# Kernel tuning notes

Measured on AMD Instinct MI355X. Metric: run time of the kernel, lower is better.

The kernel has to match this reference:

```python
import jax, jax.numpy as jnp
import numpy as np

B = 131072   # batch of states (e.g. ODE integrator batch)
S = 2        # state_dim (q, p)
H = 512      # hidden_dim
E = 8        # action_embedding_dim


def setup_inputs() -> dict:
    key = jax.random.key(0)
    ks = jax.random.split(key, 8)
    sc = lambda n: 1.0 / np.sqrt(n)
    return {
        "t": 0,  # unused time scalar (odeint signature)
        "state": jax.random.normal(ks[0], (B, S), dtype=jnp.float32),
        "action_emb": jax.random.normal(ks[1], (B, E), dtype=jnp.float32),
        # H_net: Linear(S,H) -> Softplus -> Linear(H,H) -> Softplus -> Linear(H,1)
        "W1": jax.random.normal(ks[2], (S, H), dtype=jnp.float32) * sc(S),
        "b1": jnp.zeros((H,), dtype=jnp.float32),
        "W2": jax.random.normal(ks[3], (H, H), dtype=jnp.float32) * sc(H),
        "b2": jnp.zeros((H,), dtype=jnp.float32),
        "W3": jax.random.normal(ks[4], (H, 1), dtype=jnp.float32) * sc(H),
        "b3": jnp.zeros((1,), dtype=jnp.float32),
        "log_damping": jnp.asarray(-1.0, dtype=jnp.float32),
        # G_net: Linear(E, S//2)
        "Gw": jax.random.normal(ks[5], (E, S // 2), dtype=jnp.float32) * sc(E),
        "Gb": jnp.zeros((S // 2,), dtype=jnp.float32),
    }


def reference(t, state, action_emb, W1, b1, W2, b2, W3, b3, log_damping, Gw, Gb):
    # Hamiltonian net: scalar H per state; sum over batch so jax.grad gives
    # per-sample dH/dstate in one pass (equivalent to autograd.grad with ones cotangent).
    def H_sum(s):
        h = jax.nn.softplus(s @ W1 + b1)       # [B, H]
        h = jax.nn.softplus(h @ W2 + b2)       # [B, H]
        return jnp.sum(h @ W3 + b3)            # scalar

    dH_dstate = jax.grad(H_sum)(state)         # [B, S]
    dH_dq = dH_dstate[..., 0:1]                # [B, 1]
    dH_dp = dH_dstate[..., 1:2]                # [B, 1]

    damping = jnp.exp(log_damping)
    G_u = action_emb @ Gw + Gb                 # [B, 1]

    dq_dt = dH_dp
    dp_dt = -dH_dq - damping * dH_dp + G_u
    return jnp.concatenate([dq_dt, dp_dt], axis=-1)  # [B, S]
```

## Files before the change

### kernel.cpp

```cpp
#include <hip/hip_runtime.h>

typedef __bf16 bf16x8 __attribute__((ext_vector_type(8)));
typedef float f32x4 __attribute__((ext_vector_type(4)));
typedef float f32x16 __attribute__((ext_vector_type(16)));
typedef unsigned short u16x8 __attribute__((ext_vector_type(8)));

#define DEVI static __device__ __forceinline__

DEVI unsigned short f2b(float x) {
  __bf16 b = (__bf16)x;
  return __builtin_bit_cast(unsigned short, b);
}

DEVI float ex2(float x) {
#if __has_builtin(__builtin_amdgcn_exp2f)
  return __builtin_amdgcn_exp2f(x);
#else
  return __expf(x * 0.69314718f);
#endif
}
DEVI float lg2(float x) {
#if __has_builtin(__builtin_amdgcn_logf)
  return __builtin_amdgcn_logf(x);
#else
  return __logf(x) * 1.44269504f;
#endif
}

__global__ __launch_bounds__(256) void pack_w2_kernel(
    const float* __restrict__ W2, unsigned short* __restrict__ p1,
    unsigned short* __restrict__ p2) {
  int idx = blockIdx.x * 256 + threadIdx.x;
  int which = idx >> 18;
  int i = idx & 262143;
  int j = i & 7;
  int l = (i >> 3) & 63;
  if (which == 0) {
    int t0 = (i >> 9) & 15;
    int s = i >> 13;
    p1[i] = f2b(W2[(s * 16 + (l >> 5) * 8 + j) * 512 + t0 * 32 + (l & 31)]);
  } else {
    int t0 = (i >> 9) & 31;
    int s = i >> 14;
    p2[i] = f2b(W2[(t0 * 16 + (l & 15)) * 512 + s * 32 + (l >> 4) * 8 + j]);
  }
}

__global__ __launch_bounds__(512, 4) void phm_kernel(
    const float* __restrict__ state, const float* __restrict__ action_emb,
    const float* __restrict__ W1, const float* __restrict__ b1,
    const float* __restrict__ b2, const float* __restrict__ W3,
    const float* __restrict__ log_damping, const float* __restrict__ Gw,
    const float* __restrict__ Gb, const unsigned short* __restrict__ packB1,
    const unsigned short* __restrict__ packB2, float* __restrict__ out) {
  __shared__ unsigned short buf[64 * 512];
  __shared__ float4 w1tab[512];
  __shared__ float W3s[512];
  __shared__ float st[128];
  __shared__ float2 part2[8][64];

  const int t = threadIdx.x;
  const int lane = t & 63;
  const int wid = t >> 6;
  const int l15 = lane & 15;
  const int l4 = lane >> 4;
  const int l31 = lane & 31;
  const int l5 = lane >> 5;
  const long row0 = (long)blockIdx.x * 64;
  char* bufc = reinterpret_cast<char*>(buf);
  const float LOG2E = 1.44269504f;

  if (t < 512) {
    w1tab[t] = make_float4(W1[t] * LOG2E, W1[512 + t] * LOG2E,
                           b1[t] * LOG2E, b2[t] * LOG2E);
    W3s[t] = W3[t];
  }
  if (t < 128) st[t] = state[row0 * 2 + t];
  __syncthreads();

  const float2 stA = *reinterpret_cast<const float2*>(&st[l31 * 2]);
  const float2 stB = *reinterpret_cast<const float2*>(&st[(32 + l31) * 2]);
#pragma unroll
  for (int it = 0; it < 8; ++it) {
    int page = it * 8 + wid;
    int s = page >> 1, rt = page & 1;
    float2 sp = rt ? stB : stA;
    int k0 = s * 16 + l5 * 8;
    u16x8 pk;
#pragma unroll
    for (int j = 0; j < 8; ++j) {
      float4 w = w1tab[k0 + j];
      float zp = fmaf(sp.x, w.x, fmaf(sp.y, w.y, w.z));
      float hp = fmaxf(zp, 0.f) + lg2(1.f + ex2(-fabsf(zp)));
      pk[j] = f2b(hp);
    }
    *reinterpret_cast<u16x8*>(bufc + page * 1024 + lane * 16) = pk;
  }
  __syncthreads();

  f32x16 acc1[2][2];
#pragma unroll
  for (int rt = 0; rt < 2; ++rt)
#pragma unroll
    for (int ct = 0; ct < 2; ++ct)
#pragma unroll
      for (int r = 0; r < 16; ++r) acc1[rt][ct][r] = 0.f;

#pragma unroll 4
  for (int s = 0; s < 32; ++s) {
    bf16x8 af[2];
#pragma unroll
    for (int rt = 0; rt < 2; ++rt)
      af[rt] = __builtin_bit_cast(
          bf16x8, *reinterpret_cast<const int4*>(
                      bufc + (s * 2 + rt) * 1024 + lane * 16));
    bf16x8 bfr[2];
#pragma unroll
    for (int ct = 0; ct < 2; ++ct)
      bfr[ct] = __builtin_bit_cast(
          bf16x8, *reinterpret_cast<const int4*>(
                      packB1 + ((s * 16 + wid * 2 + ct) * 64 + lane) * 8));
#pragma unroll
    for (int rt = 0; rt < 2; ++rt)
#pragma unroll
      for (int ct = 0; ct < 2; ++ct)
        acc1[rt][ct] = __builtin_amdgcn_mfma_f32_32x32x16_bf16(
            af[rt], bfr[ct], acc1[rt][ct], 0, 0, 0);
  }
  __syncthreads();

#pragma unroll
  for (int ct = 0; ct < 2; ++ct) {
    int c = (wid * 2 + ct) * 32 + l31;
    float w3 = W3s[c], bbL = w1tab[c].w;
    int pbase = (c >> 5) * 4096 + (c & 7) * 2;
    int oct = (c >> 3) & 3;
#pragma unroll
    for (int rt = 0; rt < 2; ++rt) {
#pragma unroll
      for (int reg = 0; reg < 16; ++reg) {
        int row = rt * 32 + (reg & 3) + 8 * (reg >> 2) + 4 * l5;
        float e = ex2(-(acc1[rt][ct][reg] + bbL));
        float sg = __builtin_amdgcn_rcpf(1.f + e);
        unsigned short u = f2b(w3 * sg);
        int lane2 = (row & 15) + 16 * oct;
        int slot = lane2 ^ (lane2 >> 4);
        *reinterpret_cast<unsigned short*>(
            bufc + pbase + (row >> 4) * 1024 + slot * 16) = u;
      }
    }
  }
  __syncthreads();

  float p0[16], p1v[16];
#pragma unroll
  for (int i = 0; i < 16; ++i) { p0[i] = 0.f; p1v[i] = 0.f; }

  const int rslot = (lane ^ (lane >> 4)) * 16;
#pragma unroll
  for (int chunk = 0; chunk < 2; ++chunk) {
    f32x4 acc2[4][2];
#pragma unroll
    for (int a = 0; a < 4; ++a)
#pragma unroll
      for (int b = 0; b < 2; ++b)
#pragma unroll
        for (int r = 0; r < 4; ++r) acc2[a][b][r] = 0.f;

#pragma unroll 2
    for (int s2 = 0; s2 < 16; ++s2) {
      bf16x8 af[4];
#pragma unroll
      for (int rt2 = 0; rt2 < 4; ++rt2)
        af[rt2] = __builtin_bit_cast(
            bf16x8, *reinterpret_cast<const int4*>(
                        bufc + s2 * 4096 + rt2 * 1024 + rslot));
      bf16x8 bfr[2];
#pragma unroll
      for (int cc = 0; cc < 2; ++cc)
        bfr[cc] = __builtin_bit_cast(
            bf16x8,
            *reinterpret_cast<const int4*>(
                packB2 + ((s2 * 32 + wid * 4 + chunk * 2 + cc) * 64 + lane) * 8));
#pragma unroll
      for (int rt2 = 0; rt2 < 4; ++rt2)
#pragma unroll
        for (int cc = 0; cc < 2; ++cc)
          acc2[rt2][cc] = __builtin_amdgcn_mfma_f32_16x16x32_bf16(
              af[rt2], bfr[cc], acc2[rt2][cc], 0, 0, 0);
    }
#pragma unroll
    for (int rt2 = 0; rt2 < 4; ++rt2) {
      float2 rv[4];
#pragma unroll
      for (int jj = 0; jj < 4; ++jj)
        rv[jj] = *reinterpret_cast<const float2*>(
            &st[(rt2 * 16 + l4 * 4 + jj) * 2]);
#pragma unroll
      for (int cc = 0; cc < 2; ++cc) {
        int hc = wid * 64 + (chunk * 2 + cc) * 16 + l15;
        float4 w = w1tab[hc];
        float w10L = w.x, w11L = w.y, bbL = w.z;
#pragma unroll
        for (int jj = 0; jj < 4; ++jj) {
          float z1L = fmaf(rv[jj].x, w10L, fmaf(rv[jj].y, w11L, bbL));
          float sg = __builtin_amdgcn_rcpf(1.f + ex2(-z1L));
          float dz1 = acc2[rt2][cc][jj] * sg;
          p0[rt2 * 4 + jj] = fmaf(dz1, w10L, p0[rt2 * 4 + jj]);
          p1v[rt2 * 4 + jj] = fmaf(dz1, w11L, p1v[rt2 * 4 + jj]);
        }
      }
    }
  }

  float a8[8], b8[8];
  {
    bool bb = (l15 & 1) != 0;
#pragma unroll
    for (int m = 0; m < 8; ++m) {
      float ka = bb ? p0[2 * m + 1] : p0[2 * m];
      float sa = bb ? p0[2 * m] : p0[2 * m + 1];
      a8[m] = ka + __shfl_xor(sa, 1, 64);
      float kb = bb ? p1v[2 * m + 1] : p1v[2 * m];
      float sb = bb ? p1v[2 * m] : p1v[2 * m + 1];
      b8[m] = kb + __shfl_xor(sb, 1, 64);
    }
  }
  float a4[4], b4[4];
  {
    bool bb = (l15 & 2) != 0;
#pragma unroll
    for (int m = 0; m < 4; ++m) {
      float ka = bb ? a8[2 * m + 1] : a8[2 * m];
      float sa = bb ? a8[2 * m] : a8[2 * m + 1];
      a4[m] = ka + __shfl_xor(sa, 2, 64);
      float kb = bb ? b8[2 * m + 1] : b8[2 * m];
      float sb = bb ? b8[2 * m] : b8[2 * m + 1];
      b4[m] = kb + __shfl_xor(sb, 2, 64);
    }
  }
  float a2[2], b2v[2];
  {
    bool bb = (l15 & 4) != 0;
#pragma unroll
    for (int m = 0; m < 2; ++m) {
      float ka = bb ? a4[2 * m + 1] : a4[2 * m];
      float sa = bb ? a4[2 * m] : a4[2 * m + 1];
      a2[m] = ka + __shfl_xor(sa, 4, 64);
      float kb = bb ? b4[2 * m + 1] : b4[2 * m];
      float sb = bb ? b4[2 * m] : b4[2 * m + 1];
      b2v[m] = kb + __shfl_xor(sb, 4, 64);
    }
  }
  float a1, b1r;
  {
    bool bb = (l15 & 8) != 0;
    float ka = bb ? a2[1] : a2[0];
    float sa = bb ? a2[0] : a2[1];
    a1 = ka + __shfl_xor(sa, 8, 64);
    float kb = bb ? b2v[1] : b2v[0];
    float sb = bb ? b2v[0] : b2v[1];
    b1r = kb + __shfl_xor(sb, 8, 64);
  }
  {
    int r = (l15 >> 2) * 16 + l4 * 4 + (l15 & 3);
    part2[wid][r] = make_float2(a1, b1r);
  }
  __syncthreads();

  if (t < 64) {
    long grow = row0 + t;
    float g0 = 0.f, g1 = 0.f;
#pragma unroll
    for (int w = 0; w < 8; ++w) {
      float2 pp = part2[w][t];
      g0 += pp.x;
      g1 += pp.y;
    }
    const float LN2 = 0.69314718f;
    g0 *= LN2;
    g1 *= LN2;
    const float4 ae0 = reinterpret_cast<const float4*>(action_emb)[grow * 2];
    const float4 ae1 = reinterpret_cast<const float4*>(action_emb)[grow * 2 + 1];
    float gu = Gb[0];
    gu = fmaf(ae0.x, Gw[0], gu);
    gu = fmaf(ae0.y, Gw[1], gu);
    gu = fmaf(ae0.z, Gw[2], gu);
    gu = fmaf(ae0.w, Gw[3], gu);
    gu = fmaf(ae1.x, Gw[4], gu);
    gu = fmaf(ae1.y, Gw[5], gu);
    gu = fmaf(ae1.z, Gw[6], gu);
    gu = fmaf(ae1.w, Gw[7], gu);
    float damping = __expf(log_damping[0]);
    float2 o;
    o.x = g1;
    o.y = -g0 - damping * g1 + gu;
    reinterpret_cast<float2*>(out)[grow] = o;
  }
}

extern "C" void kernel_launch(void* const* d_in, const int* in_sizes, int n_in,
                              void* d_out, int out_size, void* d_ws,
                              size_t ws_size, hipStream_t stream) {
  const float* state = (const float*)d_in[1];
  const float* action_emb = (const float*)d_in[2];
  const float* W1 = (const float*)d_in[3];
  const float* b1 = (const float*)d_in[4];
  const float* W2 = (const float*)d_in[5];
  const float* b2 = (const float*)d_in[6];
  const float* W3 = (const float*)d_in[7];
  const float* log_damping = (const float*)d_in[9];
  const float* Gw = (const float*)d_in[10];
  const float* Gb = (const float*)d_in[11];
  float* out = (float*)d_out;

  unsigned short* p1 = (unsigned short*)d_ws;
  unsigned short* p2 = p1 + 262144;

  pack_w2_kernel<<<dim3(2048), dim3(256), 0, stream>>>(W2, p1, p2);
  phm_kernel<<<dim3(2048), dim3(512), 0, stream>>>(
      state, action_emb, W1, b1, b2, W3, log_damping, Gw, Gb, p1, p2, out);
}
```

Baseline: 156.9 us.

## Double block size to 1024 threads, halving per-wave column tiles

Launches 16 waves per block instead of 8, so each wave handles one column tile in the first GEMM and one chunk per pass in the second instead of two. The partial-gradient reduction gains an extra two-phase combine through shared memory. The aim is more waves in flight to hide latency and fewer accumulator registers per wave. The cost is doubled LDS A-fragment reads across waves, an extra barrier, and a tighter register cap that may cause spills.

```diff
diff --git a/kernel.cpp b/kernel.cpp
--- a/kernel.cpp
+++ b/kernel.cpp
@@ -46,7 +46,7 @@
   }
 }
 
-__global__ __launch_bounds__(512, 4) void phm_kernel(
+__global__ __launch_bounds__(1024, 8) void phm_kernel(
     const float* __restrict__ state, const float* __restrict__ action_emb,
     const float* __restrict__ W1, const float* __restrict__ b1,
     const float* __restrict__ b2, const float* __restrict__ W3,
@@ -75,16 +75,15 @@
                            b1[t] * LOG2E, b2[t] * LOG2E);
     W3s[t] = W3[t];
   }
-  if (t < 128) st[t] = state[row0 * 2 + t];
-  __syncthreads();
-
-  const float2 stA = *reinterpret_cast<const float2*>(&st[l31 * 2]);
-  const float2 stB = *reinterpret_cast<const float2*>(&st[(32 + l31) * 2]);
-#pragma unroll
-  for (int it = 0; it < 8; ++it) {
-    int page = it * 8 + wid;
-    int s = page >> 1, rt = page & 1;
-    float2 sp = rt ? stB : stA;
+  if (t >= 512 && t < 640) st[t - 512] = state[row0 * 2 + (t - 512)];
+  __syncthreads();
+
+  const float2 sp = *reinterpret_cast<const float2*>(
+      &st[((wid & 1) * 32 + l31) * 2]);
+#pragma unroll
+  for (int it = 0; it < 4; ++it) {
+    int page = it * 16 + wid;
+    int s = page >> 1;
     int k0 = s * 16 + l5 * 8;
     u16x8 pk;
 #pragma unroll
@@ -98,13 +97,11 @@
   }
   __syncthreads();
 
-  f32x16 acc1[2][2];
+  f32x16 acc1[2];
 #pragma unroll
   for (int rt = 0; rt < 2; ++rt)
 #pragma unroll
-    for (int ct = 0; ct < 2; ++ct)
-#pragma unroll
-      for (int r = 0; r < 16; ++r) acc1[rt][ct][r] = 0.f;
+    for (int r = 0; r < 16; ++r) acc1[rt][r] = 0.f;
 
 #pragma unroll 4
   for (int s = 0; s < 32; ++s) {
@@ -114,24 +111,18 @@
       af[rt] = __builtin_bit_cast(
           bf16x8, *reinterpret_cast<const int4*>(
                       bufc + (s * 2 + rt) * 1024 + lane * 16));
-    bf16x8 bfr[2];
-#pragma unroll
-    for (int ct = 0; ct < 2; ++ct)
-      bfr[ct] = __builtin_bit_cast(
-          bf16x8, *reinterpret_cast<const int4*>(
-                      packB1 + ((s * 16 + wid * 2 + ct) * 64 + lane) * 8));
+    bf16x8 bfr = __builtin_bit_cast(
+        bf16x8, *reinterpret_cast<const int4*>(
+                    packB1 + ((s * 16 + wid) * 64 + lane) * 8));
 #pragma unroll
     for (int rt = 0; rt < 2; ++rt)
-#pragma unroll
-      for (int ct = 0; ct < 2; ++ct)
-        acc1[rt][ct] = __builtin_amdgcn_mfma_f32_32x32x16_bf16(
-            af[rt], bfr[ct], acc1[rt][ct], 0, 0, 0);
-  }
-  __syncthreads();
-
-#pragma unroll
-  for (int ct = 0; ct < 2; ++ct) {
-    int c = (wid * 2 + ct) * 32 + l31;
+      acc1[rt] = __builtin_amdgcn_mfma_f32_32x32x16_bf16(
+          af[rt], bfr, acc1[rt], 0, 0, 0);
+  }
+  __syncthreads();
+
+  {
+    int c = wid * 32 + l31;
     float w3 = W3s[c], bbL = w1tab[c].w;
     int pbase = (c >> 5) * 4096 + (c & 7) * 2;
     int oct = (c >> 3) & 3;
@@ -140,7 +131,7 @@
 #pragma unroll
       for (int reg = 0; reg < 16; ++reg) {
         int row = rt * 32 + (reg & 3) + 8 * (reg >> 2) + 4 * l5;
-        float e = ex2(-(acc1[rt][ct][reg] + bbL));
+        float e = ex2(-(acc1[rt][reg] + bbL));
         float sg = __builtin_amdgcn_rcpf(1.f + e);
         unsigned short u = f2b(w3 * sg);
         int lane2 = (row & 15) + 16 * oct;
@@ -159,13 +150,11 @@
   const int rslot = (lane ^ (lane >> 4)) * 16;
 #pragma unroll
   for (int chunk = 0; chunk < 2; ++chunk) {
-    f32x4 acc2[4][2];
+    f32x4 acc2[4];
 #pragma unroll
     for (int a = 0; a < 4; ++a)
 #pragma unroll
-      for (int b = 0; b < 2; ++b)
-#pragma unroll
-        for (int r = 0; r < 4; ++r) acc2[a][b][r] = 0.f;
+      for (int r = 0; r < 4; ++r) acc2[a][r] = 0.f;
 
 #pragma unroll 2
     for (int s2 = 0; s2 < 16; ++s2) {
@@ -175,40 +164,28 @@
         af[rt2] = __builtin_bit_cast(
             bf16x8, *reinterpret_cast<const int4*>(
                         bufc + s2 * 4096 + rt2 * 1024 + rslot));
-      bf16x8 bfr[2];
-#pragma unroll
-      for (int cc = 0; cc < 2; ++cc)
-        bfr[cc] = __builtin_bit_cast(
-            bf16x8,
-            *reinterpret_cast<const int4*>(
-                packB2 + ((s2 * 32 + wid * 4 + chunk * 2 + cc) * 64 + lane) * 8));
+      bf16x8 bfr = __builtin_bit_cast(
+          bf16x8, *reinterpret_cast<const int4*>(
+                      packB2 + ((s2 * 32 + wid * 2 + chunk) * 64 + lane) * 8));
 #pragma unroll
       for (int rt2 = 0; rt2 < 4; ++rt2)
-#pragma unroll
-        for (int cc = 0; cc < 2; ++cc)
-          acc2[rt2][cc] = __builtin_amdgcn_mfma_f32_16x16x32_bf16(
-              af[rt2], bfr[cc], acc2[rt2][cc], 0, 0, 0);
-    }
+        acc2[rt2] = __builtin_amdgcn_mfma_f32_16x16x32_bf16(
+            af[rt2], bfr, acc2[rt2], 0, 0, 0);
+    }
+    int hc = wid * 32 + chunk * 16 + l15;
+    float4 w = w1tab[hc];
+    float w10L = w.x, w11L = w.y, bbL = w.z;
 #pragma unroll
     for (int rt2 = 0; rt2 < 4; ++rt2) {
-      float2 rv[4];
-#pragma unroll
-      for (int jj = 0; jj < 4; ++jj)
-        rv[jj] = *reinterpret_cast<const float2*>(
+#pragma unroll
+      for (int jj = 0; jj < 4; ++jj) {
+        float2 rv = *reinterpret_cast<const float2*>(
             &st[(rt2 * 16 + l4 * 4 + jj) * 2]);
-#pragma unroll
-      for (int cc = 0; cc < 2; ++cc) {
-        int hc = wid * 64 + (chunk * 2 + cc) * 16 + l15;
-        float4 w = w1tab[hc];
-        float w10L = w.x, w11L = w.y, bbL = w.z;
-#pragma unroll
-        for (int jj = 0; jj < 4; ++jj) {
-          float z1L = fmaf(rv[jj].x, w10L, fmaf(rv[jj].y, w11L, bbL));
-          float sg = __builtin_amdgcn_rcpf(1.f + ex2(-z1L));
-          float dz1 = acc2[rt2][cc][jj] * sg;
-          p0[rt2 * 4 + jj] = fmaf(dz1, w10L, p0[rt2 * 4 + jj]);
-          p1v[rt2 * 4 + jj] = fmaf(dz1, w11L, p1v[rt2 * 4 + jj]);
-        }
+        float z1L = fmaf(rv.x, w10L, fmaf(rv.y, w11L, bbL));
+        float sg = __builtin_amdgcn_rcpf(1.f + ex2(-z1L));
+        float dz1 = acc2[rt2][jj] * sg;
+        p0[rt2 * 4 + jj] = fmaf(dz1, w10L, p0[rt2 * 4 + jj]);
+        p1v[rt2 * 4 + jj] = fmaf(dz1, w11L, p1v[rt2 * 4 + jj]);
       }
     }
   }
@@ -262,9 +239,12 @@
     float sb = bb ? b2v[0] : b2v[1];
     b1r = kb + __shfl_xor(sb, 8, 64);
   }
-  {
-    int r = (l15 >> 2) * 16 + l4 * 4 + (l15 & 3);
-    part2[wid][r] = make_float2(a1, b1r);
+  const int r = (l15 >> 2) * 16 + l4 * 4 + (l15 & 3);
+  if (wid < 8) part2[wid][r] = make_float2(a1, b1r);
+  __syncthreads();
+  if (wid >= 8) {
+    float2 pp = part2[wid - 8][r];
+    part2[wid - 8][r] = make_float2(pp.x + a1, pp.y + b1r);
   }
   __syncthreads();
 
@@ -318,6 +298,6 @@
   unsigned short* p2 = p1 + 262144;
 
   pack_w2_kernel<<<dim3(2048), dim3(256), 0, stream>>>(W2, p1, p2);
-  phm_kernel<<<dim3(2048), dim3(512), 0, stream>>>(
+  phm_kernel<<<dim3(2048), dim3(1024), 0, stream>>>(
       state, action_emb, W1, b1, b2, W3, log_damping, Gw, Gb, p1, p2, out);
 }
```

After: 246.9 us. +57.4%, slower.

## Halve rows per block to 32 and raise occupancy target

Applied to the files above, without the earlier changes.

Each block now processes 32 rows instead of 64, launching twice as many blocks with smaller shared memory (buf halved) and fewer accumulator registers, and launch bounds raised to 6 waves per SIMD. The MFMA tiling, LDS layout strides and shuffle-reduction tree are reworked to match the smaller row tile. The aim is more resident blocks per CU to hide latency, at the cost of reloading the packed W2 fragments from global/L2 twice as often per row, which lowers weight reuse.

```diff
diff --git a/kernel.cpp b/kernel.cpp
--- a/kernel.cpp
+++ b/kernel.cpp
@@ -46,18 +46,18 @@
   }
 }
 
-__global__ __launch_bounds__(512, 4) void phm_kernel(
+__global__ __launch_bounds__(512, 6) void phm_kernel(
     const float* __restrict__ state, const float* __restrict__ action_emb,
     const float* __restrict__ W1, const float* __restrict__ b1,
     const float* __restrict__ b2, const float* __restrict__ W3,
     const float* __restrict__ log_damping, const float* __restrict__ Gw,
     const float* __restrict__ Gb, const unsigned short* __restrict__ packB1,
     const unsigned short* __restrict__ packB2, float* __restrict__ out) {
-  __shared__ unsigned short buf[64 * 512];
+  __shared__ unsigned short buf[32 * 512];
   __shared__ float4 w1tab[512];
   __shared__ float W3s[512];
-  __shared__ float st[128];
-  __shared__ float2 part2[8][64];
+  __shared__ float st[64];
+  __shared__ float2 part2[8][32];
 
   const int t = threadIdx.x;
   const int lane = t & 63;
@@ -66,7 +66,7 @@
   const int l4 = lane >> 4;
   const int l31 = lane & 31;
   const int l5 = lane >> 5;
-  const long row0 = (long)blockIdx.x * 64;
+  const long row0 = (long)blockIdx.x * 32;
   char* bufc = reinterpret_cast<char*>(buf);
   const float LOG2E = 1.44269504f;
 
@@ -75,16 +75,13 @@
                            b1[t] * LOG2E, b2[t] * LOG2E);
     W3s[t] = W3[t];
   }
-  if (t < 128) st[t] = state[row0 * 2 + t];
-  __syncthreads();
-
-  const float2 stA = *reinterpret_cast<const float2*>(&st[l31 * 2]);
-  const float2 stB = *reinterpret_cast<const float2*>(&st[(32 + l31) * 2]);
-#pragma unroll
-  for (int it = 0; it < 8; ++it) {
-    int page = it * 8 + wid;
-    int s = page >> 1, rt = page & 1;
-    float2 sp = rt ? stB : stA;
+  if (t < 64) st[t] = state[row0 * 2 + t];
+  __syncthreads();
+
+  const float2 sp = *reinterpret_cast<const float2*>(&st[l31 * 2]);
+#pragma unroll
+  for (int it = 0; it < 4; ++it) {
+    int s = it * 8 + wid;
     int k0 = s * 16 + l5 * 8;
     u16x8 pk;
 #pragma unroll
@@ -94,26 +91,20 @@
       float hp = fmaxf(zp, 0.f) + lg2(1.f + ex2(-fabsf(zp)));
       pk[j] = f2b(hp);
     }
-    *reinterpret_cast<u16x8*>(bufc + page * 1024 + lane * 16) = pk;
-  }
-  __syncthreads();
-
-  f32x16 acc1[2][2];
-#pragma unroll
-  for (int rt = 0; rt < 2; ++rt)
-#pragma unroll
-    for (int ct = 0; ct < 2; ++ct)
-#pragma unroll
-      for (int r = 0; r < 16; ++r) acc1[rt][ct][r] = 0.f;
+    *reinterpret_cast<u16x8*>(bufc + s * 1024 + lane * 16) = pk;
+  }
+  __syncthreads();
+
+  f32x16 acc1[2];
+#pragma unroll
+  for (int ct = 0; ct < 2; ++ct)
+#pragma unroll
+    for (int r = 0; r < 16; ++r) acc1[ct][r] = 0.f;
 
 #pragma unroll 4
   for (int s = 0; s < 32; ++s) {
-    bf16x8 af[2];
-#pragma unroll
-    for (int rt = 0; rt < 2; ++rt)
-      af[rt] = __builtin_bit_cast(
-          bf16x8, *reinterpret_cast<const int4*>(
-                      bufc + (s * 2 + rt) * 1024 + lane * 16));
+    bf16x8 af = __builtin_bit_cast(
+        bf16x8, *reinterpret_cast<const int4*>(bufc + s * 1024 + lane * 16));
     bf16x8 bfr[2];
 #pragma unroll
     for (int ct = 0; ct < 2; ++ct)
@@ -121,47 +112,42 @@
           bf16x8, *reinterpret_cast<const int4*>(
                       packB1 + ((s * 16 + wid * 2 + ct) * 64 + lane) * 8));
 #pragma unroll
-    for (int rt = 0; rt < 2; ++rt)
-#pragma unroll
-      for (int ct = 0; ct < 2; ++ct)
-        acc1[rt][ct] = __builtin_amdgcn_mfma_f32_32x32x16_bf16(
-            af[rt], bfr[ct], acc1[rt][ct], 0, 0, 0);
+    for (int ct = 0; ct < 2; ++ct)
+      acc1[ct] = __builtin_amdgcn_mfma_f32_32x32x16_bf16(
+          af, bfr[ct], acc1[ct], 0, 0, 0);
   }
   __syncthreads();
 
 #pragma unroll
   for (int ct = 0; ct < 2; ++ct) {
-    int c = (wid * 2 + ct) * 32 + l31;
+    int c = wid * 64 + ct * 32 + l31;
     float w3 = W3s[c], bbL = w1tab[c].w;
-    int pbase = (c >> 5) * 4096 + (c & 7) * 2;
+    int pbase = (c >> 5) * 2048 + (c & 7) * 2;
     int oct = (c >> 3) & 3;
 #pragma unroll
-    for (int rt = 0; rt < 2; ++rt) {
-#pragma unroll
-      for (int reg = 0; reg < 16; ++reg) {
-        int row = rt * 32 + (reg & 3) + 8 * (reg >> 2) + 4 * l5;
-        float e = ex2(-(acc1[rt][ct][reg] + bbL));
-        float sg = __builtin_amdgcn_rcpf(1.f + e);
-        unsigned short u = f2b(w3 * sg);
-        int lane2 = (row & 15) + 16 * oct;
-        int slot = lane2 ^ (lane2 >> 4);
-        *reinterpret_cast<unsigned short*>(
-            bufc + pbase + (row >> 4) * 1024 + slot * 16) = u;
-      }
-    }
-  }
-  __syncthreads();
-
-  float p0[16], p1v[16];
-#pragma unroll
-  for (int i = 0; i < 16; ++i) { p0[i] = 0.f; p1v[i] = 0.f; }
+    for (int reg = 0; reg < 16; ++reg) {
+      int row = (reg & 3) + 8 * (reg >> 2) + 4 * l5;
+      float e = ex2(-(acc1[ct][reg] + bbL));
+      float sg = __builtin_amdgcn_rcpf(1.f + e);
+      unsigned short u = f2b(w3 * sg);
+      int lane2 = (row & 15) + 16 * oct;
+      int slot = lane2 ^ (lane2 >> 4);
+      *reinterpret_cast<unsigned short*>(
+          bufc + pbase + (row >> 4) * 1024 + slot * 16) = u;
+    }
+  }
+  __syncthreads();
+
+  float p0[8], p1v[8];
+#pragma unroll
+  for (int i = 0; i < 8; ++i) { p0[i] = 0.f; p1v[i] = 0.f; }
 
   const int rslot = (lane ^ (lane >> 4)) * 16;
 #pragma unroll
   for (int chunk = 0; chunk < 2; ++chunk) {
-    f32x4 acc2[4][2];
-#pragma unroll
-    for (int a = 0; a < 4; ++a)
+    f32x4 acc2[2][2];
+#pragma unroll
+    for (int a = 0; a < 2; ++a)
 #pragma unroll
       for (int b = 0; b < 2; ++b)
 #pragma unroll
@@ -169,12 +155,12 @@
 
 #pragma unroll 2
     for (int s2 = 0; s2 < 16; ++s2) {
-      bf16x8 af[4];
-#pragma unroll
-      for (int rt2 = 0; rt2 < 4; ++rt2)
+      bf16x8 af[2];
+#pragma unroll
+      for (int rt2 = 0; rt2 < 2; ++rt2)
         af[rt2] = __builtin_bit_cast(
             bf16x8, *reinterpret_cast<const int4*>(
-                        bufc + s2 * 4096 + rt2 * 1024 + rslot));
+                        bufc + s2 * 2048 + rt2 * 1024 + rslot));
       bf16x8 bfr[2];
 #pragma unroll
       for (int cc = 0; cc < 2; ++cc)
@@ -183,27 +169,24 @@
             *reinterpret_cast<const int4*>(
                 packB2 + ((s2 * 32 + wid * 4 + chunk * 2 + cc) * 64 + lane) * 8));
 #pragma unroll
-      for (int rt2 = 0; rt2 < 4; ++rt2)
+      for (int rt2 = 0; rt2 < 2; ++rt2)
 #pragma unroll
         for (int cc = 0; cc < 2; ++cc)
           acc2[rt2][cc] = __builtin_amdgcn_mfma_f32_16x16x32_bf16(
               af[rt2], bfr[cc], acc2[rt2][cc], 0, 0, 0);
     }
 #pragma unroll
-    for (int rt2 = 0; rt2 < 4; ++rt2) {
-      float2 rv[4];
-#pragma unroll
-      for (int jj = 0; jj < 4; ++jj)
-        rv[jj] = *reinterpret_cast<const float2*>(
-            &st[(rt2 * 16 + l4 * 4 + jj) * 2]);
+    for (int rt2 = 0; rt2 < 2; ++rt2) {
 #pragma unroll
       for (int cc = 0; cc < 2; ++cc) {
-        int hc = wid * 64 + (chunk * 2 + cc) * 16 + l15;
+        int hc = wid * 64 + chunk * 32 + cc * 16 + l15;
         float4 w = w1tab[hc];
         float w10L = w.x, w11L = w.y, bbL = w.z;
 #pragma unroll
         for (int jj = 0; jj < 4; ++jj) {
-          float z1L = fmaf(rv[jj].x, w10L, fmaf(rv[jj].y, w11L, bbL));
+          float2 rv = *reinterpret_cast<const float2*>(
+              &st[(rt2 * 16 + l4 * 4 + jj) * 2]);
+          float z1L = fmaf(rv.x, w10L, fmaf(rv.y, w11L, bbL));
           float sg = __builtin_amdgcn_rcpf(1.f + ex2(-z1L));
           float dz1 = acc2[rt2][cc][jj] * sg;
           p0[rt2 * 4 + jj] = fmaf(dz1, w10L, p0[rt2 * 4 + jj]);
@@ -213,62 +196,51 @@
     }
   }
 
-  float a8[8], b8[8];
+  float a4[4], b4[4];
   {
     bool bb = (l15 & 1) != 0;
 #pragma unroll
-    for (int m = 0; m < 8; ++m) {
+    for (int m = 0; m < 4; ++m) {
       float ka = bb ? p0[2 * m + 1] : p0[2 * m];
       float sa = bb ? p0[2 * m] : p0[2 * m + 1];
-      a8[m] = ka + __shfl_xor(sa, 1, 64);
+      a4[m] = ka + __shfl_xor(sa, 1, 64);
       float kb = bb ? p1v[2 * m + 1] : p1v[2 * m];
       float sb = bb ? p1v[2 * m] : p1v[2 * m + 1];
-      b8[m] = kb + __shfl_xor(sb, 1, 64);
-    }
-  }
-  float a4[4], b4[4];
+      b4[m] = kb + __shfl_xor(sb, 1, 64);
+    }
+  }
+  float a2[2], b2v[2];
   {
     bool bb = (l15 & 2) != 0;
-#pragma unroll
-    for (int m = 0; m < 4; ++m) {
-      float ka = bb ? a8[2 * m + 1] : a8[2 * m];
-      float sa = bb ? a8[2 * m] : a8[2 * m + 1];
-      a4[m] = ka + __shfl_xor(sa, 2, 64);
-      float kb = bb ? b8[2 * m + 1] : b8[2 * m];
-      float sb = bb ? b8[2 * m] : b8[2 * m + 1];
-      b4[m] = kb + __shfl_xor(sb, 2, 64);
-    }
-  }
-  float a2[2], b2v[2];
-  {
-    bool bb = (l15 & 4) != 0;
 #pragma unroll
     for (int m = 0; m < 2; ++m) {
       float ka = bb ? a4[2 * m + 1] : a4[2 * m];
       float sa = bb ? a4[2 * m] : a4[2 * m + 1];
-      a2[m] = ka + __shfl_xor(sa, 4, 64);
+      a2[m] = ka + __shfl_xor(sa, 2, 64);
       float kb = bb ? b4[2 * m + 1] : b4[2 * m];
       float sb = bb ? b4[2 * m] : b4[2 * m + 1];
-      b2v[m] = kb + __shfl_xor(sb, 4, 64);
+      b2v[m] = kb + __shfl_xor(sb, 2, 64);
     }
   }
   float a1, b1r;
   {
-    bool bb = (l15 & 8) != 0;
+    bool bb = (l15 & 4) != 0;
     float ka = bb ? a2[1] : a2[0];
     float sa = bb ? a2[0] : a2[1];
-    a1 = ka + __shfl_xor(sa, 8, 64);
+    a1 = ka + __shfl_xor(sa, 4, 64);
     float kb = bb ? b2v[1] : b2v[0];
     float sb = bb ? b2v[0] : b2v[1];
-    b1r = kb + __shfl_xor(sb, 8, 64);
-  }
-  {
-    int r = (l15 >> 2) * 16 + l4 * 4 + (l15 & 3);
+    b1r = kb + __shfl_xor(sb, 4, 64);
+  }
+  a1 += __shfl_xor(a1, 8, 64);
+  b1r += __shfl_xor(b1r, 8, 64);
+  if ((l15 & 8) == 0) {
+    int r = ((l15 >> 2) & 1) * 16 + l4 * 4 + (l15 & 3);
     part2[wid][r] = make_float2(a1, b1r);
   }
   __syncthreads();
 
-  if (t < 64) {
+  if (t < 32) {
     long grow = row0 + t;
     float g0 = 0.f, g1 = 0.f;
 #pragma unroll
@@ -318,6 +290,6 @@
   unsigned short* p2 = p1 + 262144;
 
   pack_w2_kernel<<<dim3(2048), dim3(256), 0, stream>>>(W2, p1, p2);
-  phm_kernel<<<dim3(2048), dim3(512), 0, stream>>>(
+  phm_kernel<<<dim3(4096), dim3(512), 0, stream>>>(
       state, action_emb, W1, b1, b2, W3, log_damping, Gw, Gb, p1, p2, out);
 }
```

Measured after the change: 195.6 us. 1.25x slower.
